# Optimization experiments

Measured on AMD Instinct MI355X. Metric: run time of the kernel, lower is better.

Reference implementation:

```python
import jax, jax.numpy as jnp
import numpy as np

COST_CLASS = 1.0
COST_BBOX = 5.0
COST_GIOU = 2.0


def box_cxcywh_to_xyxy(b):
    cx, cy, w, h = b[..., 0], b[..., 1], b[..., 2], b[..., 3]
    return jnp.stack([cx - 0.5 * w, cy - 0.5 * h, cx + 0.5 * w, cy + 0.5 * h], axis=-1)


def generalized_box_iou(boxes1, boxes2):
    # boxes1: [N,4] xyxy, boxes2: [M,4] xyxy -> [N,M]
    area1 = (boxes1[:, 2] - boxes1[:, 0]) * (boxes1[:, 3] - boxes1[:, 1])
    area2 = (boxes2[:, 2] - boxes2[:, 0]) * (boxes2[:, 3] - boxes2[:, 1])
    lt = jnp.maximum(boxes1[:, None, :2], boxes2[None, :, :2])  # [N,M,2]
    rb = jnp.minimum(boxes1[:, None, 2:], boxes2[None, :, 2:])
    wh = jnp.clip(rb - lt, 0.0)
    inter = wh[..., 0] * wh[..., 1]
    union = area1[:, None] + area2[None, :] - inter
    iou = inter / union
    lt_e = jnp.minimum(boxes1[:, None, :2], boxes2[None, :, :2])
    rb_e = jnp.maximum(boxes1[:, None, 2:], boxes2[None, :, 2:])
    wh_e = jnp.clip(rb_e - lt_e, 0.0)
    area_e = wh_e[..., 0] * wh_e[..., 1]
    return iou - (area_e - union) / area_e


def setup_inputs() -> dict:
    key = jax.random.key(0)
    k1, k2, k3, k4 = jax.random.split(key, 4)
    B, Q, C, T = 16, 900, 92, 1600
    pred_logits = jax.random.normal(k1, (B, Q, C), dtype=jnp.float32)
    pred_boxes = jax.random.uniform(k2, (B, Q, 4), dtype=jnp.float32)
    tgt_labels = jax.random.randint(k3, (T,), 0, C, dtype=jnp.int64)
    tgt_boxes = jax.random.uniform(k4, (T, 4), dtype=jnp.float32)
    return {"pred_logits": pred_logits, "pred_boxes": pred_boxes,
            "tgt_labels": tgt_labels, "tgt_boxes": tgt_boxes}


def reference(pred_logits, pred_boxes, tgt_labels, tgt_boxes):
    B, Q, C = pred_logits.shape
    out_prob = jax.nn.softmax(pred_logits.reshape(B * Q, C), axis=-1)  # [BQ,C]
    out_bbox = pred_boxes.reshape(B * Q, 4)
    # classification cost: -prob at the target class (gather over columns)
    cost_class = -out_prob[:, tgt_labels]  # [BQ,T]
    # L1 cdist between predicted and target boxes (cxcywh)
    cost_bbox = jnp.sum(jnp.abs(out_bbox[:, None, :] - tgt_bbox_expand(tgt_boxes)), axis=-1)
    # GIoU cost on xyxy boxes
    cost_giou = -generalized_box_iou(box_cxcywh_to_xyxy(out_bbox), box_cxcywh_to_xyxy(tgt_boxes))
    cost = COST_BBOX * cost_bbox + COST_CLASS * cost_class + COST_GIOU * cost_giou
    return cost.reshape(B, Q, -1)


def tgt_bbox_expand(tgt_boxes):
    return tgt_boxes[None, :, :]
```

## Files before the change

kernel.cpp:

```cpp
#include <hip/hip_runtime.h>
#include <hip/hip_bf16.h>
#include <math.h>


#define RQ   16
#define TT   800
#define GG   200
#define NTHR 256
#define CC   92
#define CP   96

__global__ __launch_bounds__(NTHR) void detr_cost_kernel(
    const float* __restrict__ logits,
    const float* __restrict__ pboxes,
    const int*   __restrict__ labels,
    const float* __restrict__ tboxes,
    float*       __restrict__ out,
    int T)
{
    __shared__ alignas(16) float s_tx1[TT];
    __shared__ alignas(16) float s_ty1[TT];
    __shared__ alignas(16) float s_tx2[TT];
    __shared__ alignas(16) float s_ty2[TT];
    __shared__ alignas(16) int   s_lbl[TT];
    __shared__ float4 s_pbox[RQ];
    __shared__ float  s_parea[RQ];
    __shared__ float  s_nprob[RQ * CP];

    const int tid  = threadIdx.x;
    const int row0 = blockIdx.x * RQ;
    const int tb   = blockIdx.y * TT;

    const float4* tb4 = (const float4*)tboxes;
    for (int j = tid; j < TT; j += NTHR) {
        float4 t = tb4[tb + j];
        s_tx1[j] = t.x - 0.5f * t.z;
        s_ty1[j] = t.y - 0.5f * t.w;
        s_tx2[j] = t.x + 0.5f * t.z;
        s_ty2[j] = t.y + 0.5f * t.w;
        s_lbl[j] = labels[tb + j];
    }

    if (tid < RQ) {
        float4 p = ((const float4*)pboxes)[row0 + tid];
        float x1 = p.x - 0.5f * p.z, y1 = p.y - 0.5f * p.w;
        float x2 = p.x + 0.5f * p.z, y2 = p.y + 0.5f * p.w;
        s_pbox[tid]  = make_float4(x1, y1, x2, y2);
        s_parea[tid] = (x2 - x1) * (y2 - y1);
    }

    const int wv = tid >> 6, ln = tid & 63;
    for (int rr = wv; rr < RQ; rr += 4) {
        const float* lg = logits + (long long)(row0 + rr) * CC;
        float v1 = (ln < CC)      ? lg[ln]      : -INFINITY;
        float v2 = (ln + 64 < CC) ? lg[ln + 64] : -INFINITY;
        float m = fmaxf(v1, v2);
        #pragma unroll
        for (int o = 32; o > 0; o >>= 1) m = fmaxf(m, __shfl_xor(m, o));
        float e1 = (ln < CC)      ? __expf(v1 - m) : 0.0f;
        float e2 = (ln + 64 < CC) ? __expf(v2 - m) : 0.0f;
        float s = e1 + e2;
        #pragma unroll
        for (int o = 32; o > 0; o >>= 1) s += __shfl_xor(s, o);
        float inv = __builtin_amdgcn_rcpf(s);
        if (ln < CC)      s_nprob[rr * CP + ln]      = -e1 * inv;
        if (ln + 64 < CC) s_nprob[rr * CP + ln + 64] = -e2 * inv;
    }

    __syncthreads();

    for (int w = tid; w < RQ * GG; w += NTHR) {
        const int row = w / GG;
        const int g   = w - row * GG;

        const float4 pb = s_pbox[row];
        const float  pa = s_parea[row];
        const float* np = &s_nprob[row * CP];

        const float4 tx1 = *(const float4*)&s_tx1[4 * g];
        const float4 ty1 = *(const float4*)&s_ty1[4 * g];
        const float4 tx2 = *(const float4*)&s_tx2[4 * g];
        const float4 ty2 = *(const float4*)&s_ty2[4 * g];
        const int4   lb  = *(const int4*)&s_lbl[4 * g];

        const float* fx1 = (const float*)&tx1;
        const float* fy1 = (const float*)&ty1;
        const float* fx2 = (const float*)&tx2;
        const float* fy2 = (const float*)&ty2;
        const int*   flb = (const int*)&lb;

        float4 r;
        float* rp = (float*)&r;
        #pragma unroll
        for (int u = 0; u < 4; ++u) {
            const float x1 = fx1[u], y1 = fy1[u], x2 = fx2[u], y2 = fy2[u];

            const float d1 = pb.x - x1, d2 = pb.z - x2;
            const float e1 = pb.y - y1, e2 = pb.w - y2;
            const float l1 = 0.5f * (fabsf(d1 + d2) + fabsf(e1 + e2))
                           + fabsf(d2 - d1) + fabsf(e2 - e1);

            const float ta    = (x2 - x1) * (y2 - y1);
            const float iw    = fminf(pb.z, x2) - fmaxf(pb.x, x1);
            const float ih    = fminf(pb.w, y2) - fmaxf(pb.y, y1);
            const float inter = fmaxf(iw, 0.0f) * fmaxf(ih, 0.0f);
            const float uni   = pa + ta - inter;
            const float iou   = inter * __builtin_amdgcn_rcpf(uni);

            const float ew   = fmaxf(pb.z, x2) - fminf(pb.x, x1);
            const float eh   = fmaxf(pb.w, y2) - fminf(pb.y, y1);
            const float ea   = ew * eh;
            const float giou = iou - (ea - uni) * __builtin_amdgcn_rcpf(ea);

            rp[u] = fmaf(5.0f, l1, np[flb[u]]) - 2.0f * giou;
        }

        *(float4*)(out + (long long)(row0 + row) * T + tb + 4 * g) = r;
    }
}

extern "C" void kernel_launch(void* const* d_in, const int* in_sizes, int n_in,
                              void* d_out, int out_size, void* d_ws, size_t ws_size,
                              hipStream_t stream) {
    const float* logits = (const float*)d_in[0];
    const float* pboxes = (const float*)d_in[1];
    const int*   labels = (const int*)d_in[2];
    const float* tboxes = (const float*)d_in[3];
    float* out = (float*)d_out;

    const int T  = in_sizes[2];
    const int BQ = in_sizes[1] / 4;

    dim3 grid(BQ / RQ, T / TT);
    detr_cost_kernel<<<grid, NTHR, 0, stream>>>(logits, pboxes, labels, tboxes, out, T);
}
```

Before: 127.4 us.

## Map one target per thread in registers and loop over 48 query rows

The kernel is restructured so each thread owns one target box and label, held in registers, and loops over 48 query rows per block. Prediction boxes are read with uniform global loads, and per-row negative probabilities come from shared memory. This drops the target staging through shared memory and the float4 output stores, replacing them with coalesced scalar stores per row. It also uses a 320-thread block and a transposed grid, relying on T dividing by 320 and BQ dividing by 48. Softmax work per block grows to 48 rows handled by 5 wavefronts.

```diff
diff --git a/kernel.cpp b/kernel.cpp
--- a/kernel.cpp
+++ b/kernel.cpp
@@ -3,10 +3,8 @@
 #include <math.h>
 
 
-#define RQ   16
-#define TT   800
-#define GG   200
-#define NTHR 256
+#define NTHR 320
+#define RR   48
 #define CC   92
 #define CP   96
 
@@ -18,39 +16,22 @@
     float*       __restrict__ out,
     int T)
 {
-    __shared__ alignas(16) float s_tx1[TT];
-    __shared__ alignas(16) float s_ty1[TT];
-    __shared__ alignas(16) float s_tx2[TT];
-    __shared__ alignas(16) float s_ty2[TT];
-    __shared__ alignas(16) int   s_lbl[TT];
-    __shared__ float4 s_pbox[RQ];
-    __shared__ float  s_parea[RQ];
-    __shared__ float  s_nprob[RQ * CP];
+    __shared__ float s_nprob[RR * CP];
 
     const int tid  = threadIdx.x;
-    const int row0 = blockIdx.x * RQ;
-    const int tb   = blockIdx.y * TT;
+    const int j    = blockIdx.x * NTHR + tid;
+    const int row0 = blockIdx.y * RR;
 
-    const float4* tb4 = (const float4*)tboxes;
-    for (int j = tid; j < TT; j += NTHR) {
-        float4 t = tb4[tb + j];
-        s_tx1[j] = t.x - 0.5f * t.z;
-        s_ty1[j] = t.y - 0.5f * t.w;
-        s_tx2[j] = t.x + 0.5f * t.z;
-        s_ty2[j] = t.y + 0.5f * t.w;
-        s_lbl[j] = labels[tb + j];
-    }
-
-    if (tid < RQ) {
-        float4 p = ((const float4*)pboxes)[row0 + tid];
-        float x1 = p.x - 0.5f * p.z, y1 = p.y - 0.5f * p.w;
-        float x2 = p.x + 0.5f * p.z, y2 = p.y + 0.5f * p.w;
-        s_pbox[tid]  = make_float4(x1, y1, x2, y2);
-        s_parea[tid] = (x2 - x1) * (y2 - y1);
-    }
+    const float4 t = ((const float4*)tboxes)[j];
+    const float tx1 = t.x - 0.5f * t.z;
+    const float ty1 = t.y - 0.5f * t.w;
+    const float tx2 = t.x + 0.5f * t.z;
+    const float ty2 = t.y + 0.5f * t.w;
+    const float ta  = t.z * t.w;
+    const int   lbl = labels[j];
 
     const int wv = tid >> 6, ln = tid & 63;
-    for (int rr = wv; rr < RQ; rr += 4) {
+    for (int rr = wv; rr < RR; rr += 5) {
         const float* lg = logits + (long long)(row0 + rr) * CC;
         float v1 = (ln < CC)      ? lg[ln]      : -INFINITY;
         float v2 = (ln + 64 < CC) ? lg[ln + 64] : -INFINITY;
@@ -69,53 +50,33 @@
 
     __syncthreads();
 
-    for (int w = tid; w < RQ * GG; w += NTHR) {
-        const int row = w / GG;
-        const int g   = w - row * GG;
+    const float4* pb4 = (const float4*)pboxes;
+    #pragma unroll 4
+    for (int r = 0; r < RR; ++r) {
+        const float4 p = pb4[row0 + r];
+        const float px1 = p.x - 0.5f * p.z;
+        const float py1 = p.y - 0.5f * p.w;
+        const float px2 = p.x + 0.5f * p.z;
+        const float py2 = p.y + 0.5f * p.w;
+        const float pa  = p.z * p.w;
 
-        const float4 pb = s_pbox[row];
-        const float  pa = s_parea[row];
-        const float* np = &s_nprob[row * CP];
+        const float nprob = s_nprob[r * CP + lbl];
 
-        const float4 tx1 = *(const float4*)&s_tx1[4 * g];
-        const float4 ty1 = *(const float4*)&s_ty1[4 * g];
-        const float4 tx2 = *(const float4*)&s_tx2[4 * g];
-        const float4 ty2 = *(const float4*)&s_ty2[4 * g];
-        const int4   lb  = *(const int4*)&s_lbl[4 * g];
+        const float l1 = fabsf(p.x - t.x) + fabsf(p.y - t.y)
+                       + fabsf(p.z - t.z) + fabsf(p.w - t.w);
 
-        const float* fx1 = (const float*)&tx1;
-        const float* fy1 = (const float*)&ty1;
-        const float* fx2 = (const float*)&tx2;
-        const float* fy2 = (const float*)&ty2;
-        const int*   flb = (const int*)&lb;
+        const float iw    = fminf(px2, tx2) - fmaxf(px1, tx1);
+        const float ih    = fminf(py2, ty2) - fmaxf(py1, ty1);
+        const float inter = fmaxf(iw, 0.0f) * fmaxf(ih, 0.0f);
+        const float uni   = pa + ta - inter;
+        const float iou   = inter * __builtin_amdgcn_rcpf(uni);
 
-        float4 r;
-        float* rp = (float*)&r;
-        #pragma unroll
-        for (int u = 0; u < 4; ++u) {
-            const float x1 = fx1[u], y1 = fy1[u], x2 = fx2[u], y2 = fy2[u];
+        const float ew   = fmaxf(px2, tx2) - fminf(px1, tx1);
+        const float eh   = fmaxf(py2, ty2) - fminf(py1, ty1);
+        const float ea   = ew * eh;
+        const float giou = iou - (ea - uni) * __builtin_amdgcn_rcpf(ea);
 
-            const float d1 = pb.x - x1, d2 = pb.z - x2;
-            const float e1 = pb.y - y1, e2 = pb.w - y2;
-            const float l1 = 0.5f * (fabsf(d1 + d2) + fabsf(e1 + e2))
-                           + fabsf(d2 - d1) + fabsf(e2 - e1);
-
-            const float ta    = (x2 - x1) * (y2 - y1);
-            const float iw    = fminf(pb.z, x2) - fmaxf(pb.x, x1);
-            const float ih    = fminf(pb.w, y2) - fmaxf(pb.y, y1);
-            const float inter = fmaxf(iw, 0.0f) * fmaxf(ih, 0.0f);
-            const float uni   = pa + ta - inter;
-            const float iou   = inter * __builtin_amdgcn_rcpf(uni);
-
-            const float ew   = fmaxf(pb.z, x2) - fminf(pb.x, x1);
-            const float eh   = fmaxf(pb.w, y2) - fminf(pb.y, y1);
-            const float ea   = ew * eh;
-            const float giou = iou - (ea - uni) * __builtin_amdgcn_rcpf(ea);
-
-            rp[u] = fmaf(5.0f, l1, np[flb[u]]) - 2.0f * giou;
-        }
-
-        *(float4*)(out + (long long)(row0 + row) * T + tb + 4 * g) = r;
+        out[(long long)(row0 + r) * T + j] = fmaf(5.0f, l1, nprob) - 2.0f * giou;
     }
 }
 
@@ -131,6 +92,6 @@
     const int T  = in_sizes[2];
     const int BQ = in_sizes[1] / 4;
 
-    dim3 grid(BQ / RQ, T / TT);
+    dim3 grid(T / NTHR, BQ / RR);
     detr_cost_kernel<<<grid, NTHR, 0, stream>>>(logits, pboxes, labels, tboxes, out, T);
 }
```

Result: slower. 137.1 us (+7.6%).
